# Kernel tuning notes

Measured on AMD Instinct MI355X. Metric: run time of the kernel, lower is better.

The kernel has to match this reference:

```python
import jax, jax.numpy as jnp
import numpy as np

B, V, D = 32768, 2, 512   # batch, views (code hard-codes 2 via cat(subject, subject)), hidden dim
S, L = 32, 8              # number of subjects, number of labels -> K = S*L groups
DENS_TEMP = 0.1           # args.Intersubsim_dens_temp (temperature/base_temperature are unused in forward)


def setup_inputs() -> dict:
    key = jax.random.key(0)
    k1, k2, k3 = jax.random.split(key, 3)
    X_data = jax.random.normal(k1, (B, V, D), dtype=jnp.float32)
    subject = jax.random.randint(k2, (B,), 0, S, dtype=jnp.int32)
    labels = jax.random.randint(k3, (B,), 0, L, dtype=jnp.int32)
    return {"X_data": X_data, "subject": subject, "labels": labels}


def reference(X_data, subject, labels):
    K = S * L
    # contrast_feature = cat(unbind(X_data, dim=1), dim=0): view-major stacking -> [V*B, D]
    feat = jnp.concatenate([X_data[:, v, :] for v in range(V)], axis=0)
    sub2 = jnp.concatenate([subject, subject])   # subject_ten
    lab2 = jnp.concatenate([labels, labels])     # labels_ten

    # group id per row; loop order (sorted unique subject, sorted unique label) == s*L + l
    gid = sub2 * L + lab2                         # [2B]
    counts = jax.ops.segment_sum(jnp.ones(gid.shape, feat.dtype), gid, K)   # [K]
    sums = jax.ops.segment_sum(feat, gid, K)                                 # [K, D]
    centroid = sums / counts[:, None]                                        # per-group mean

    # per-point euclidean distance to own-group centroid (torch.cdist)
    dist = jnp.sqrt(jnp.sum((feat - centroid[gid]) ** 2, axis=1))            # [2B]
    # density: mean(dist ** 0.5) / log(n_g + 10) for groups with >1 member
    mean_sqrt = jax.ops.segment_sum(jnp.sqrt(dist), gid, K) / counts
    dens = mean_sqrt / jnp.log(counts + 10.0)
    dmax = jnp.max(jnp.where(counts > 1, dens, -jnp.inf))
    density = jnp.where(counts > 1, dens, dmax)
    density = jnp.clip(density, jnp.quantile(density, 0.1), jnp.quantile(density, 0.9))
    density = DENS_TEMP * density / density.mean()
    # torch path goes through .tolist() -> density carries no gradient
    density = jax.lax.stop_gradient(density)

    # masks: positives = same label, different subject (group index equals raw id here)
    g_sub = jnp.arange(K, dtype=sub2.dtype) // L
    g_lab = jnp.arange(K, dtype=lab2.dtype) % L
    mask = ((sub2[:, None] != g_sub[None, :]) & (lab2[:, None] == g_lab[None, :])).astype(feat.dtype)  # [2B, K]
    # with S>=2 and all labels present, every row has at least one positive -> no row drop

    sim = (feat @ centroid.T) / density[None, :]          # [2B, K]
    sim = sim - jnp.max(sim, axis=1, keepdims=True)
    positive_sim = sim * mask
    # CrossEntropyLoss with soft (unnormalized) float targets: -sum target*log_softmax
    logp = jax.nn.log_softmax(positive_sim, axis=1)
    loss = -jnp.sum(mask * logp, axis=1) / jnp.sum(mask, axis=1)
    return loss.mean()
```

## Files before the change

kernel.cpp:

```cpp
#include <hip/hip_runtime.h>
#include <math.h>

#define BN 32768
#define DN 512
#define SN 32
#define LN 8
#define KN 256
#define N2 65536
#define SPLIT 8

typedef __attribute__((ext_vector_type(8))) short bf16x8;
typedef __attribute__((ext_vector_type(4))) float f32x4;

#define OFF_XBF     0ull
#define OFF_PART    67108864ull
#define OFF_SUMS    71303168ull
#define OFF_CENTB   71827456ull
#define OFF_GID     72089600ull
#define OFF_PERM    72220672ull
#define OFF_BASE    72351744ull
#define OFF_OFFW    72352772ull
#define OFF_COUNTS  72353796ull
#define OFF_SUMQ    72354820ull
#define OFF_INVD    72355844ull
#define OFF_LOSS    72356868ull
#define ZERO_OFF    OFF_COUNTS
#define ZERO_BYTES  (72356872ull - OFF_COUNTS)

__device__ __forceinline__ float atomAddF(float* p, float v) {
  return unsafeAtomicAdd(p, v);
}

__device__ __forceinline__ ushort f2bf(float x) {
  union { float f; unsigned u; } v; v.f = x;
  unsigned u = v.u;
  unsigned r = (u + 0x7fffu + ((u >> 16) & 1u)) >> 16;
  return (ushort)r;
}

__device__ __forceinline__ float bf2f(ushort x) {
  union { unsigned u; float f; } v; v.u = ((unsigned)x) << 16;
  return v.f;
}

__device__ __forceinline__ void async16(const void* g, void* l) {
  __builtin_amdgcn_global_load_lds(
      (const __attribute__((address_space(1))) unsigned int*)g,
      (__attribute__((address_space(3))) unsigned int*)l, 16, 0, 0);
}

__global__ __launch_bounds__(256) void k0_gid(const int* __restrict__ subject,
    const int* __restrict__ labels, int* __restrict__ gid, int* __restrict__ counts) {
  __shared__ int hist[KN];
  hist[threadIdx.x] = 0;
  __syncthreads();
  const int b0 = blockIdx.x * 1024;
  for (int i = threadIdx.x; i < 1024; i += 256) {
    int b = b0 + i;
    int g = subject[b] * LN + labels[b];
    gid[b] = g;
    atomicAdd(&hist[g], 1);
  }
  __syncthreads();
  if (hist[threadIdx.x]) atomicAdd(&counts[threadIdx.x], 2 * hist[threadIdx.x]);
}

__global__ __launch_bounds__(256) void k0b_scan(const int* __restrict__ counts,
    int* __restrict__ base, int* __restrict__ offw) {
  __shared__ int sh[KN];
  const int t = threadIdx.x;
  const int h = counts[t] >> 1;
  sh[t] = h;
  __syncthreads();
  for (int d = 1; d < 256; d <<= 1) {
    int add = (t >= d) ? sh[t - d] : 0;
    __syncthreads();
    sh[t] += add;
    __syncthreads();
  }
  const int excl = sh[t] - h;
  base[t] = excl;
  offw[t] = excl;
  if (t == 255) base[256] = sh[255];
}

__global__ __launch_bounds__(256) void k0c_scatter(const int* __restrict__ gid,
    int* __restrict__ offw, int* __restrict__ perm) {
  __shared__ int lhist[KN];
  __shared__ int lbase[KN];
  const int t = threadIdx.x;
  const int b0 = blockIdx.x * 1024;
  lhist[t] = 0;
  __syncthreads();
  int g[4], lr[4];
#pragma unroll
  for (int k = 0; k < 4; ++k) {
    g[k] = gid[b0 + k * 256 + t];
    lr[k] = atomicAdd(&lhist[g[k]], 1);
  }
  __syncthreads();
  const int h = lhist[t];
  if (h) lbase[t] = atomicAdd(&offw[t], h);
  __syncthreads();
#pragma unroll
  for (int k = 0; k < 4; ++k) {
    perm[lbase[g[k]] + lr[k]] = b0 + k * 256 + t;
  }
}

__global__ __launch_bounds__(256) void k1_sums(const float* __restrict__ X,
    const int* __restrict__ perm, const int* __restrict__ base,
    ushort* __restrict__ Xb, float* __restrict__ partial) {
  __shared__ float buf[4 * 512];
  const int g = blockIdx.x >> 3;
  const int s = blockIdx.x & (SPLIT - 1);
  const int t = threadIdx.x;
  const int w = t >> 6;
  const int lane = t & 63;
  const int start = base[g], end = base[g + 1];
  const int vs = s * 4 + w;

  float4 a0 = {0.f, 0.f, 0.f, 0.f};
  float4 a1 = {0.f, 0.f, 0.f, 0.f};

  int i = start + vs;
  if (i < end) {
    int idx = perm[i];
    const float* bp = X + (size_t)idx * 1024 + lane * 4;
    float4 x0 = *(const float4*)(bp);
    float4 x1 = *(const float4*)(bp + 256);
    float4 x2 = *(const float4*)(bp + 512);
    float4 x3 = *(const float4*)(bp + 768);
    while (true) {
      const int inext = i + 32;
      int idxn = idx;
      float4 y0 = x0, y1 = x1, y2 = x2, y3 = x3;
      if (inext < end) {
        idxn = perm[inext];
        const float* bn = X + (size_t)idxn * 1024 + lane * 4;
        y0 = *(const float4*)(bn);
        y1 = *(const float4*)(bn + 256);
        y2 = *(const float4*)(bn + 512);
        y3 = *(const float4*)(bn + 768);
      }
      a0.x += x0.x + x2.x; a0.y += x0.y + x2.y;
      a0.z += x0.z + x2.z; a0.w += x0.w + x2.w;
      a1.x += x1.x + x3.x; a1.y += x1.y + x3.y;
      a1.z += x1.z + x3.z; a1.w += x1.w + x3.w;
      ushort* xb0 = Xb + (size_t)idx * DN + lane * 4;
      ushort* xb1 = Xb + (size_t)(idx + BN) * DN + lane * 4;
      *(ushort4*)(xb0)       = (ushort4){f2bf(x0.x), f2bf(x0.y), f2bf(x0.z), f2bf(x0.w)};
      *(ushort4*)(xb0 + 256) = (ushort4){f2bf(x1.x), f2bf(x1.y), f2bf(x1.z), f2bf(x1.w)};
      *(ushort4*)(xb1)       = (ushort4){f2bf(x2.x), f2bf(x2.y), f2bf(x2.z), f2bf(x2.w)};
      *(ushort4*)(xb1 + 256) = (ushort4){f2bf(x3.x), f2bf(x3.y), f2bf(x3.z), f2bf(x3.w)};
      if (inext >= end) break;
      i = inext; idx = idxn; x0 = y0; x1 = y1; x2 = y2; x3 = y3;
    }
  }
  *(float4*)&buf[w * 512 + lane * 4] = a0;
  *(float4*)&buf[w * 512 + 256 + lane * 4] = a1;
  __syncthreads();
  if (t < 128) {
    float4 r = {0.f, 0.f, 0.f, 0.f};
#pragma unroll
    for (int ww = 0; ww < 4; ++ww) {
      float4 v = *(float4*)&buf[ww * 512 + t * 4];
      r.x += v.x; r.y += v.y; r.z += v.z; r.w += v.w;
    }
    *(float4*)&partial[((size_t)s * KN + g) * DN + t * 4] = r;
  }
}

__global__ __launch_bounds__(256) void k1b_cent(const float* __restrict__ partial,
    const int* __restrict__ counts, float* __restrict__ sums,
    ushort* __restrict__ centB) {
  const int i = blockIdx.x * 256 + threadIdx.x;
  const int g = i >> 9;
  float ss = 0.f;
#pragma unroll
  for (int s = 0; s < SPLIT; ++s) ss += partial[(size_t)s * (KN * DN) + i];
  sums[i] = ss;
  centB[i] = f2bf(ss / (float)counts[g]);
}

__global__ __launch_bounds__(256) void k3_dist(const ushort* __restrict__ Xb,
    const int* __restrict__ perm, const int* __restrict__ base,
    const float* __restrict__ sums, const int* __restrict__ counts,
    float* __restrict__ sumq) {
  __shared__ float wacc[4];
  const int g = blockIdx.x >> 3;
  const int s = blockIdx.x & (SPLIT - 1);
  const int t = threadIdx.x;
  const int w = t >> 6;
  const int lane = t & 63;
  const int start = base[g], end = base[g + 1];
  const int nviews = 2 * (end - start);
  const float invc = 1.0f / (float)counts[g];
  const float* sp = sums + g * DN + lane * 8;
  float4 c0 = *(const float4*)sp;
  float4 c1 = *(const float4*)(sp + 4);
  const float cs[8] = {c0.x * invc, c0.y * invc, c0.z * invc, c0.w * invc,
                       c1.x * invc, c1.y * invc, c1.z * invc, c1.w * invc};
  float q = 0.f;
  const int vs = s * 4 + w;
  for (int j = vs; j < nviews; j += SPLIT * 4) {
    const int idx = perm[start + (j >> 1)];
    const int row = idx + (j & 1) * BN;
    int4 chunk = *(const int4*)(Xb + (size_t)row * DN + lane * 8);
    const ushort* us = (const ushort*)&chunk;
    float ss = 0.f;
#pragma unroll
    for (int k = 0; k < 8; ++k) {
      float diff = bf2f(us[k]) - cs[k];
      ss += diff * diff;
    }
#pragma unroll
    for (int off = 32; off > 0; off >>= 1) ss += __shfl_down(ss, off, 64);
    if (lane == 0) q += sqrtf(sqrtf(ss));
  }
  if (lane == 0) wacc[w] = q;
  __syncthreads();
  if (t == 0) atomAddF(&sumq[g], wacc[0] + wacc[1] + wacc[2] + wacc[3]);
}

__global__ __launch_bounds__(256) void k4_density(const float* __restrict__ sumq,
    const int* __restrict__ counts, float* __restrict__ invd) {
  __shared__ float sv[256];
  __shared__ float st[256];
  const int t = threadIdx.x;
  const int cnt = counts[t];
  const bool valid = cnt > 1;
  float dens = 0.f;
  if (valid) dens = (sumq[t] / (float)cnt) / logf((float)cnt + 10.f);
  sv[t] = valid ? dens : -INFINITY;
  __syncthreads();
  for (int s = 128; s > 0; s >>= 1) {
    if (t < s) sv[t] = fmaxf(sv[t], sv[t + s]);
    __syncthreads();
  }
  const float dmax = sv[0];
  __syncthreads();
  const float d0 = valid ? dens : dmax;
  sv[t] = d0;
  __syncthreads();
  int rank = 0;
  for (int j = 0; j < 256; ++j) {
    float vj = sv[j];
    rank += (vj < d0) || (vj == d0 && j < t);
  }
  st[rank] = d0;
  __syncthreads();
  const float q10 = 0.5f * (st[25] + st[26]);
  const float q90 = 0.5f * (st[229] + st[230]);
  const float dc = fminf(fmaxf(d0, q10), q90);
  sv[t] = dc;
  __syncthreads();
  for (int s = 128; s > 0; s >>= 1) {
    if (t < s) sv[t] += sv[t + s];
    __syncthreads();
  }
  const float mean = sv[0] * (1.0f / 256.f);
  invd[t] = mean / (0.1f * dc);
}

#define TAB (128 * 128)
#define TBB (256 * 128)
__global__ __launch_bounds__(256, 2) void k5_mfma(const ushort* __restrict__ Xb,
    const ushort* __restrict__ centB, const int* __restrict__ subject,
    const int* __restrict__ labels, const float* __restrict__ invd,
    float* __restrict__ losssum) {
  __shared__ char smem[TAB + TBB + 1024];
  char* ldsA = smem;
  char* ldsB = smem + TAB;
  float* maxbuf = (float*)smem;
  float* gmax = (float*)(smem + 2048);
  float* ebuf = (float*)(smem + 2560);
  float* zbuf = (float*)(smem + 4608);
  int* labs = (int*)(smem + TAB + TBB);
  int* subs = labs + 128;

  const int t = threadIdx.x;
  const int w = t >> 6;
  const int lane = t & 63;
  const int quad = lane >> 4;
  const int n16 = lane & 15;
  const int li = lane >> 3;
  const int lc = lane & 7;
  const int srcc = lc ^ li;
  const int rowbase = blockIdx.x * 128;

  if (t < 128) {
    int b = (rowbase + t) & (BN - 1);
    labs[t] = labels[b];
    subs[t] = subject[b];
  }

  f32x4 acc[8][4];
#pragma unroll
  for (int mt = 0; mt < 8; ++mt)
#pragma unroll
    for (int nt = 0; nt < 4; ++nt) acc[mt][nt] = (f32x4){0.f, 0.f, 0.f, 0.f};

  const ushort* Arow = Xb + (size_t)rowbase * DN;

  for (int k0 = 0; k0 < DN; k0 += 64) {
    __syncthreads();
#pragma unroll
    for (int q = 0; q < 4; ++q) {
      const int r0 = w * 32 + q * 8;
      async16(Arow + (size_t)(r0 + li) * DN + k0 + srcc * 8, ldsA + r0 * 128);
    }
#pragma unroll
    for (int q = 0; q < 8; ++q) {
      const int g0 = w * 64 + q * 8;
      async16(centB + (size_t)(g0 + li) * DN + k0 + srcc * 8, ldsB + g0 * 128);
    }
    __syncthreads();
#pragma unroll
    for (int s = 0; s < 2; ++s) {
      const int csw = ((s * 4 + quad) ^ (n16 & 7)) * 16;
      bf16x8 bfr[4];
#pragma unroll
      for (int nt = 0; nt < 4; ++nt) {
        int g = w * 64 + nt * 16 + n16;
        bfr[nt] = *(bf16x8*)(ldsB + g * 128 + csw);
      }
#pragma unroll
      for (int mt = 0; mt < 8; ++mt) {
        bf16x8 afr = *(bf16x8*)(ldsA + (mt * 16 + n16) * 128 + csw);
#pragma unroll
        for (int nt = 0; nt < 4; ++nt)
          acc[mt][nt] = __builtin_amdgcn_mfma_f32_16x16x32_bf16(afr, bfr[nt], acc[mt][nt], 0, 0, 0);
      }
    }
  }

  float iv[4];
#pragma unroll
  for (int nt = 0; nt < 4; ++nt) iv[nt] = invd[w * 64 + nt * 16 + n16];

  __syncthreads();

#pragma unroll
  for (int mt = 0; mt < 8; ++mt) {
#pragma unroll
    for (int r = 0; r < 4; ++r) {
      float mm = -INFINITY;
#pragma unroll
      for (int nt = 0; nt < 4; ++nt) mm = fmaxf(mm, acc[mt][nt][r] * iv[nt]);
#pragma unroll
      for (int off = 1; off < 16; off <<= 1) mm = fmaxf(mm, __shfl_xor(mm, off, 64));
      if (n16 == 0) maxbuf[w * 128 + mt * 16 + quad * 4 + r] = mm;
    }
  }
  __syncthreads();
  if (t < 128)
    gmax[t] = fmaxf(fmaxf(maxbuf[t], maxbuf[128 + t]),
                    fmaxf(maxbuf[256 + t], maxbuf[384 + t]));
  __syncthreads();

#pragma unroll
  for (int mt = 0; mt < 8; ++mt) {
#pragma unroll
    for (int r = 0; r < 4; ++r) {
      const int row = mt * 16 + quad * 4 + r;
      const float gm = gmax[row];
      const int lab = labs[row];
      const int sub = subs[row];
      float e = 0.f, z = 0.f;
      if ((n16 & 7) == lab) {
#pragma unroll
        for (int nt = 0; nt < 4; ++nt) {
          int gdiv8 = w * 8 + nt * 2 + (n16 >> 3);
          if (gdiv8 != sub) {
            float sv = acc[mt][nt][r] * iv[nt] - gm;
            e += expf(sv);
            z += sv;
          }
        }
      }
#pragma unroll
      for (int off = 1; off < 16; off <<= 1) {
        e += __shfl_xor(e, off, 64);
        z += __shfl_xor(z, off, 64);
      }
      if (n16 == 0) {
        ebuf[w * 128 + row] = e;
        zbuf[w * 128 + row] = z;
      }
    }
  }
  __syncthreads();

  float lsum = 0.f;
  if (t < 128) {
    float e = ebuf[t] + ebuf[128 + t] + ebuf[256 + t] + ebuf[384 + t];
    float z = zbuf[t] + zbuf[128 + t] + zbuf[256 + t] + zbuf[384 + t];
    lsum = logf(225.f + e) - z * (1.0f / 31.0f);
  }
#pragma unroll
  for (int off = 32; off > 0; off >>= 1) lsum += __shfl_down(lsum, off, 64);
  if (lane == 0 && lsum != 0.f) atomAddF(losssum, lsum);
}

__global__ void k6_final(const float* __restrict__ losssum, float* __restrict__ out) {
  out[0] = losssum[0] * (1.0f / (float)N2);
}

extern "C" void kernel_launch(void* const* d_in, const int* in_sizes, int n_in,
                              void* d_out, int out_size, void* d_ws, size_t ws_size,
                              hipStream_t stream) {
  const float* X = (const float*)d_in[0];
  const int* subject = (const int*)d_in[1];
  const int* labels = (const int*)d_in[2];
  char* ws = (char*)d_ws;
  ushort* Xb = (ushort*)(ws + OFF_XBF);
  float* partial = (float*)(ws + OFF_PART);
  float* sums = (float*)(ws + OFF_SUMS);
  ushort* centB = (ushort*)(ws + OFF_CENTB);
  int* gid = (int*)(ws + OFF_GID);
  int* perm = (int*)(ws + OFF_PERM);
  int* basep = (int*)(ws + OFF_BASE);
  int* offw = (int*)(ws + OFF_OFFW);
  int* counts = (int*)(ws + OFF_COUNTS);
  float* sumq = (float*)(ws + OFF_SUMQ);
  float* invd = (float*)(ws + OFF_INVD);
  float* losssum = (float*)(ws + OFF_LOSS);

  hipMemsetAsync(ws + ZERO_OFF, 0, ZERO_BYTES, stream);
  k0_gid<<<BN / 1024, 256, 0, stream>>>(subject, labels, gid, counts);
  k0b_scan<<<1, 256, 0, stream>>>(counts, basep, offw);
  k0c_scatter<<<BN / 1024, 256, 0, stream>>>(gid, offw, perm);
  k1_sums<<<KN * SPLIT, 256, 0, stream>>>(X, perm, basep, Xb, partial);
  k1b_cent<<<(KN * DN) / 256, 256, 0, stream>>>(partial, counts, sums, centB);
  k3_dist<<<KN * SPLIT, 256, 0, stream>>>(Xb, perm, basep, sums, counts, sumq);
  k4_density<<<1, 256, 0, stream>>>(sumq, counts, invd);
  k5_mfma<<<N2 / 128, 256, 0, stream>>>(Xb, centB, subject, labels, invd, losssum);
  k6_final<<<1, 1, 0, stream>>>(losssum, (float*)d_out);
}
```

Baseline: 296.1 us.

## Fuse setup kernels and compute distances from the GEMM via norm expansion

Merges the gid, scan and scatter kernels into one kernel that uses a software grid barrier. It drops the separate distance pass by computing squared distance as |x|^2 - 2x·c + |c|^2, reusing the MFMA dot products plus per-row and per-centroid norms. The density and final-loss kernels are folded into the MFMA kernel behind grid barriers. This removes several launches and a full reread of the bf16 features, but relies on all 512 blocks being co-resident to avoid deadlock, and the norm expansion can lose precision to cancellation.

```diff
diff --git a/kernel.cpp b/kernel.cpp
--- a/kernel.cpp
+++ b/kernel.cpp
@@ -14,21 +14,39 @@
 
 #define OFF_XBF     0ull
 #define OFF_PART    67108864ull
-#define OFF_SUMS    71303168ull
-#define OFF_CENTB   71827456ull
-#define OFF_GID     72089600ull
-#define OFF_PERM    72220672ull
-#define OFF_BASE    72351744ull
-#define OFF_OFFW    72352772ull
-#define OFF_COUNTS  72353796ull
-#define OFF_SUMQ    72354820ull
-#define OFF_INVD    72355844ull
-#define OFF_LOSS    72356868ull
-#define ZERO_OFF    OFF_COUNTS
-#define ZERO_BYTES  (72356872ull - OFF_COUNTS)
+#define OFF_CENTB   71303168ull
+#define OFF_XNORM   71565312ull
+#define OFF_PERM    71827456ull
+#define OFF_BASE    71958528ull
+#define OFF_OFFW    71959556ull
+#define OFF_COUNTS  71960580ull
+#define OFF_SUMQ    71961604ull
+#define OFF_CNORM   71962628ull
+#define OFF_LOSS    71963652ull
+#define OFF_BARS    71963656ull
+#define ZERO_OFF    OFF_OFFW
+#define ZERO_BYTES  (71963680ull - OFF_OFFW)
 
 __device__ __forceinline__ float atomAddF(float* p, float v) {
   return unsafeAtomicAdd(p, v);
+}
+
+__device__ __forceinline__ void gridbar1(unsigned* cnt, unsigned* flag, unsigned nblocks) {
+  __syncthreads();
+  if (threadIdx.x == 0) {
+    __threadfence();
+    unsigned a = __hip_atomic_fetch_add(cnt, 1u, __ATOMIC_ACQ_REL,
+                                        __HIP_MEMORY_SCOPE_AGENT);
+    if (a + 1u == nblocks) {
+      __hip_atomic_store(flag, 1u, __ATOMIC_RELEASE, __HIP_MEMORY_SCOPE_AGENT);
+    } else {
+      while (!__hip_atomic_load(flag, __ATOMIC_ACQUIRE, __HIP_MEMORY_SCOPE_AGENT)) {
+        __builtin_amdgcn_s_sleep(2);
+      }
+    }
+    __threadfence();
+  }
+  __syncthreads();
 }
 
 __device__ __forceinline__ ushort f2bf(float x) {
@@ -49,44 +67,11 @@
       (__attribute__((address_space(3))) unsigned int*)l, 16, 0, 0);
 }
 
-__global__ __launch_bounds__(256) void k0_gid(const int* __restrict__ subject,
-    const int* __restrict__ labels, int* __restrict__ gid, int* __restrict__ counts) {
-  __shared__ int hist[KN];
-  hist[threadIdx.x] = 0;
-  __syncthreads();
-  const int b0 = blockIdx.x * 1024;
-  for (int i = threadIdx.x; i < 1024; i += 256) {
-    int b = b0 + i;
-    int g = subject[b] * LN + labels[b];
-    gid[b] = g;
-    atomicAdd(&hist[g], 1);
-  }
-  __syncthreads();
-  if (hist[threadIdx.x]) atomicAdd(&counts[threadIdx.x], 2 * hist[threadIdx.x]);
-}
-
-__global__ __launch_bounds__(256) void k0b_scan(const int* __restrict__ counts,
-    int* __restrict__ base, int* __restrict__ offw) {
+__global__ __launch_bounds__(256) void k0_all(const int* __restrict__ subject,
+    const int* __restrict__ labels, int* __restrict__ counts, int* __restrict__ base,
+    int* __restrict__ offw, int* __restrict__ perm, unsigned* __restrict__ bars) {
+  __shared__ int lhist[KN];
   __shared__ int sh[KN];
-  const int t = threadIdx.x;
-  const int h = counts[t] >> 1;
-  sh[t] = h;
-  __syncthreads();
-  for (int d = 1; d < 256; d <<= 1) {
-    int add = (t >= d) ? sh[t - d] : 0;
-    __syncthreads();
-    sh[t] += add;
-    __syncthreads();
-  }
-  const int excl = sh[t] - h;
-  base[t] = excl;
-  offw[t] = excl;
-  if (t == 255) base[256] = sh[255];
-}
-
-__global__ __launch_bounds__(256) void k0c_scatter(const int* __restrict__ gid,
-    int* __restrict__ offw, int* __restrict__ perm) {
-  __shared__ int lhist[KN];
   __shared__ int lbase[KN];
   const int t = threadIdx.x;
   const int b0 = blockIdx.x * 1024;
@@ -95,22 +80,39 @@
   int g[4], lr[4];
 #pragma unroll
   for (int k = 0; k < 4; ++k) {
-    g[k] = gid[b0 + k * 256 + t];
+    const int b = b0 + k * 256 + t;
+    g[k] = subject[b] * LN + labels[b];
     lr[k] = atomicAdd(&lhist[g[k]], 1);
   }
   __syncthreads();
   const int h = lhist[t];
-  if (h) lbase[t] = atomicAdd(&offw[t], h);
-  __syncthreads();
-#pragma unroll
-  for (int k = 0; k < 4; ++k) {
+  if (h) atomicAdd(&counts[t], 2 * h);
+  gridbar1(&bars[0], &bars[1], 32);
+  const int rows = ((int)__hip_atomic_load((unsigned*)&counts[t], __ATOMIC_RELAXED,
+                                           __HIP_MEMORY_SCOPE_AGENT)) >> 1;
+  sh[t] = rows;
+  __syncthreads();
+  for (int d = 1; d < 256; d <<= 1) {
+    int add = (t >= d) ? sh[t - d] : 0;
+    __syncthreads();
+    sh[t] += add;
+    __syncthreads();
+  }
+  const int excl = sh[t] - rows;
+  if (blockIdx.x == 0) {
+    base[t] = excl;
+    if (t == 255) base[256] = sh[255];
+  }
+  if (h) lbase[t] = excl + atomicAdd(&offw[t], h);
+  __syncthreads();
+#pragma unroll
+  for (int k = 0; k < 4; ++k)
     perm[lbase[g[k]] + lr[k]] = b0 + k * 256 + t;
-  }
 }
 
 __global__ __launch_bounds__(256) void k1_sums(const float* __restrict__ X,
     const int* __restrict__ perm, const int* __restrict__ base,
-    ushort* __restrict__ Xb, float* __restrict__ partial) {
+    ushort* __restrict__ Xb, float* __restrict__ partial, float* __restrict__ xnorm) {
   __shared__ float buf[4 * 512];
   const int g = blockIdx.x >> 3;
   const int s = blockIdx.x & (SPLIT - 1);
@@ -147,12 +149,31 @@
       a0.z += x0.z + x2.z; a0.w += x0.w + x2.w;
       a1.x += x1.x + x3.x; a1.y += x1.y + x3.y;
       a1.z += x1.z + x3.z; a1.w += x1.w + x3.w;
+      ushort4 u0 = (ushort4){f2bf(x0.x), f2bf(x0.y), f2bf(x0.z), f2bf(x0.w)};
+      ushort4 u1 = (ushort4){f2bf(x1.x), f2bf(x1.y), f2bf(x1.z), f2bf(x1.w)};
+      ushort4 u2 = (ushort4){f2bf(x2.x), f2bf(x2.y), f2bf(x2.z), f2bf(x2.w)};
+      ushort4 u3 = (ushort4){f2bf(x3.x), f2bf(x3.y), f2bf(x3.z), f2bf(x3.w)};
       ushort* xb0 = Xb + (size_t)idx * DN + lane * 4;
       ushort* xb1 = Xb + (size_t)(idx + BN) * DN + lane * 4;
-      *(ushort4*)(xb0)       = (ushort4){f2bf(x0.x), f2bf(x0.y), f2bf(x0.z), f2bf(x0.w)};
-      *(ushort4*)(xb0 + 256) = (ushort4){f2bf(x1.x), f2bf(x1.y), f2bf(x1.z), f2bf(x1.w)};
-      *(ushort4*)(xb1)       = (ushort4){f2bf(x2.x), f2bf(x2.y), f2bf(x2.z), f2bf(x2.w)};
-      *(ushort4*)(xb1 + 256) = (ushort4){f2bf(x3.x), f2bf(x3.y), f2bf(x3.z), f2bf(x3.w)};
+      *(ushort4*)(xb0)       = u0;
+      *(ushort4*)(xb0 + 256) = u1;
+      *(ushort4*)(xb1)       = u2;
+      *(ushort4*)(xb1 + 256) = u3;
+      float n0, n1, tv;
+      tv = bf2f(u0.x); n0  = tv * tv;  tv = bf2f(u0.y); n0 += tv * tv;
+      tv = bf2f(u0.z); n0 += tv * tv;  tv = bf2f(u0.w); n0 += tv * tv;
+      tv = bf2f(u1.x); n0 += tv * tv;  tv = bf2f(u1.y); n0 += tv * tv;
+      tv = bf2f(u1.z); n0 += tv * tv;  tv = bf2f(u1.w); n0 += tv * tv;
+      tv = bf2f(u2.x); n1  = tv * tv;  tv = bf2f(u2.y); n1 += tv * tv;
+      tv = bf2f(u2.z); n1 += tv * tv;  tv = bf2f(u2.w); n1 += tv * tv;
+      tv = bf2f(u3.x); n1 += tv * tv;  tv = bf2f(u3.y); n1 += tv * tv;
+      tv = bf2f(u3.z); n1 += tv * tv;  tv = bf2f(u3.w); n1 += tv * tv;
+#pragma unroll
+      for (int off = 32; off > 0; off >>= 1) {
+        n0 += __shfl_down(n0, off, 64);
+        n1 += __shfl_down(n1, off, 64);
+      }
+      if (lane == 0) { xnorm[idx] = n0; xnorm[idx + BN] = n1; }
       if (inext >= end) break;
       i = inext; idx = idxn; x0 = y0; x1 = y1; x2 = y2; x3 = y3;
     }
@@ -172,103 +193,36 @@
 }
 
 __global__ __launch_bounds__(256) void k1b_cent(const float* __restrict__ partial,
-    const int* __restrict__ counts, float* __restrict__ sums,
-    ushort* __restrict__ centB) {
-  const int i = blockIdx.x * 256 + threadIdx.x;
-  const int g = i >> 9;
-  float ss = 0.f;
-#pragma unroll
-  for (int s = 0; s < SPLIT; ++s) ss += partial[(size_t)s * (KN * DN) + i];
-  sums[i] = ss;
-  centB[i] = f2bf(ss / (float)counts[g]);
-}
-
-__global__ __launch_bounds__(256) void k3_dist(const ushort* __restrict__ Xb,
-    const int* __restrict__ perm, const int* __restrict__ base,
-    const float* __restrict__ sums, const int* __restrict__ counts,
-    float* __restrict__ sumq) {
-  __shared__ float wacc[4];
-  const int g = blockIdx.x >> 3;
-  const int s = blockIdx.x & (SPLIT - 1);
+    const int* __restrict__ counts, ushort* __restrict__ centB,
+    float* __restrict__ cnorm) {
+  __shared__ float wsum[4];
   const int t = threadIdx.x;
   const int w = t >> 6;
   const int lane = t & 63;
-  const int start = base[g], end = base[g + 1];
-  const int nviews = 2 * (end - start);
-  const float invc = 1.0f / (float)counts[g];
-  const float* sp = sums + g * DN + lane * 8;
-  float4 c0 = *(const float4*)sp;
-  float4 c1 = *(const float4*)(sp + 4);
-  const float cs[8] = {c0.x * invc, c0.y * invc, c0.z * invc, c0.w * invc,
-                       c1.x * invc, c1.y * invc, c1.z * invc, c1.w * invc};
-  float q = 0.f;
-  const int vs = s * 4 + w;
-  for (int j = vs; j < nviews; j += SPLIT * 4) {
-    const int idx = perm[start + (j >> 1)];
-    const int row = idx + (j & 1) * BN;
-    int4 chunk = *(const int4*)(Xb + (size_t)row * DN + lane * 8);
-    const ushort* us = (const ushort*)&chunk;
-    float ss = 0.f;
-#pragma unroll
-    for (int k = 0; k < 8; ++k) {
-      float diff = bf2f(us[k]) - cs[k];
-      ss += diff * diff;
-    }
-#pragma unroll
-    for (int off = 32; off > 0; off >>= 1) ss += __shfl_down(ss, off, 64);
-    if (lane == 0) q += sqrtf(sqrtf(ss));
-  }
-  if (lane == 0) wacc[w] = q;
-  __syncthreads();
-  if (t == 0) atomAddF(&sumq[g], wacc[0] + wacc[1] + wacc[2] + wacc[3]);
-}
-
-__global__ __launch_bounds__(256) void k4_density(const float* __restrict__ sumq,
-    const int* __restrict__ counts, float* __restrict__ invd) {
-  __shared__ float sv[256];
-  __shared__ float st[256];
-  const int t = threadIdx.x;
-  const int cnt = counts[t];
-  const bool valid = cnt > 1;
-  float dens = 0.f;
-  if (valid) dens = (sumq[t] / (float)cnt) / logf((float)cnt + 10.f);
-  sv[t] = valid ? dens : -INFINITY;
-  __syncthreads();
-  for (int s = 128; s > 0; s >>= 1) {
-    if (t < s) sv[t] = fmaxf(sv[t], sv[t + s]);
-    __syncthreads();
-  }
-  const float dmax = sv[0];
-  __syncthreads();
-  const float d0 = valid ? dens : dmax;
-  sv[t] = d0;
-  __syncthreads();
-  int rank = 0;
-  for (int j = 0; j < 256; ++j) {
-    float vj = sv[j];
-    rank += (vj < d0) || (vj == d0 && j < t);
-  }
-  st[rank] = d0;
-  __syncthreads();
-  const float q10 = 0.5f * (st[25] + st[26]);
-  const float q90 = 0.5f * (st[229] + st[230]);
-  const float dc = fminf(fmaxf(d0, q10), q90);
-  sv[t] = dc;
-  __syncthreads();
-  for (int s = 128; s > 0; s >>= 1) {
-    if (t < s) sv[t] += sv[t + s];
-    __syncthreads();
-  }
-  const float mean = sv[0] * (1.0f / 256.f);
-  invd[t] = mean / (0.1f * dc);
+  const int i = blockIdx.x * 256 + t;
+  const int g = i >> 9;
+  float ss = 0.f;
+#pragma unroll
+  for (int s = 0; s < SPLIT; ++s) ss += partial[(size_t)s * (KN * DN) + i];
+  const ushort cb = f2bf(ss / (float)counts[g]);
+  centB[i] = cb;
+  const float cf = bf2f(cb);
+  float c2 = cf * cf;
+#pragma unroll
+  for (int off = 32; off > 0; off >>= 1) c2 += __shfl_down(c2, off, 64);
+  if (lane == 0) wsum[w] = c2;
+  __syncthreads();
+  if (t == 0) atomAddF(&cnorm[g], wsum[0] + wsum[1] + wsum[2] + wsum[3]);
 }
 
 #define TAB (128 * 128)
 #define TBB (256 * 128)
 __global__ __launch_bounds__(256, 2) void k5_mfma(const ushort* __restrict__ Xb,
     const ushort* __restrict__ centB, const int* __restrict__ subject,
-    const int* __restrict__ labels, const float* __restrict__ invd,
-    float* __restrict__ losssum) {
+    const int* __restrict__ labels, const float* __restrict__ xnorm,
+    const float* __restrict__ cnorm, const int* __restrict__ counts,
+    float* __restrict__ sumq, float* __restrict__ losssum,
+    float* __restrict__ out, unsigned* __restrict__ bars) {
   __shared__ char smem[TAB + TBB + 1024];
   char* ldsA = smem;
   char* ldsB = smem + TAB;
@@ -276,6 +230,9 @@
   float* gmax = (float*)(smem + 2048);
   float* ebuf = (float*)(smem + 2560);
   float* zbuf = (float*)(smem + 4608);
+  float* sv   = (float*)(smem + 9216);
+  float* stv  = (float*)(smem + 10240);
+  float* dinv = (float*)(smem + 11264);
   int* labs = (int*)(smem + TAB + TBB);
   int* subs = labs + 128;
 
@@ -335,10 +292,64 @@
     }
   }
 
+#pragma unroll
+  for (int mt = 0; mt < 8; ++mt) {
+#pragma unroll
+    for (int r = 0; r < 4; ++r) {
+      const int row = mt * 16 + quad * 4 + r;
+      const int g = subs[row] * LN + labs[row];
+      if ((g >> 6) == w && (g & 15) == n16) {
+        const int nt = (g >> 4) & 3;
+        float dot = (nt == 0) ? acc[mt][0][r] : (nt == 1) ? acc[mt][1][r]
+                  : (nt == 2) ? acc[mt][2][r] : acc[mt][3][r];
+        float d2 = xnorm[rowbase + row] - 2.0f * dot + cnorm[g];
+        atomAddF(&sumq[g], sqrtf(sqrtf(fmaxf(d2, 0.0f))));
+      }
+    }
+  }
+  gridbar1(&bars[2], &bars[3], 512);
+
+  {
+    const int cnt = counts[t];
+    const bool valid = cnt > 1;
+    const float sq = __hip_atomic_load(&sumq[t], __ATOMIC_RELAXED,
+                                       __HIP_MEMORY_SCOPE_AGENT);
+    float dens = 0.f;
+    if (valid) dens = (sq / (float)cnt) / logf((float)cnt + 10.f);
+    sv[t] = valid ? dens : -INFINITY;
+    __syncthreads();
+    for (int s2 = 128; s2 > 0; s2 >>= 1) {
+      if (t < s2) sv[t] = fmaxf(sv[t], sv[t + s2]);
+      __syncthreads();
+    }
+    const float dmax = sv[0];
+    __syncthreads();
+    const float d0 = valid ? dens : dmax;
+    sv[t] = d0;
+    __syncthreads();
+    int rank = 0;
+    for (int j = 0; j < 256; ++j) {
+      float vj = sv[j];
+      rank += (vj < d0) || (vj == d0 && j < t);
+    }
+    stv[rank] = d0;
+    __syncthreads();
+    const float q10 = 0.5f * (stv[25] + stv[26]);
+    const float q90 = 0.5f * (stv[229] + stv[230]);
+    const float dc = fminf(fmaxf(d0, q10), q90);
+    sv[t] = dc;
+    __syncthreads();
+    for (int s2 = 128; s2 > 0; s2 >>= 1) {
+      if (t < s2) sv[t] += sv[t + s2];
+      __syncthreads();
+    }
+    dinv[t] = (sv[0] * (1.0f / 256.f)) / (0.1f * dc);
+  }
+  __syncthreads();
+
   float iv[4];
 #pragma unroll
-  for (int nt = 0; nt < 4; ++nt) iv[nt] = invd[w * 64 + nt * 16 + n16];
-
+  for (int nt = 0; nt < 4; ++nt) iv[nt] = dinv[w * 64 + nt * 16 + n16];
   __syncthreads();
 
 #pragma unroll
@@ -373,9 +384,9 @@
         for (int nt = 0; nt < 4; ++nt) {
           int gdiv8 = w * 8 + nt * 2 + (n16 >> 3);
           if (gdiv8 != sub) {
-            float sv = acc[mt][nt][r] * iv[nt] - gm;
-            e += expf(sv);
-            z += sv;
+            float svv = acc[mt][nt][r] * iv[nt] - gm;
+            e += expf(svv);
+            z += svv;
           }
         }
       }
@@ -401,10 +412,13 @@
 #pragma unroll
   for (int off = 32; off > 0; off >>= 1) lsum += __shfl_down(lsum, off, 64);
   if (lane == 0 && lsum != 0.f) atomAddF(losssum, lsum);
-}
-
-__global__ void k6_final(const float* __restrict__ losssum, float* __restrict__ out) {
-  out[0] = losssum[0] * (1.0f / (float)N2);
+
+  gridbar1(&bars[4], &bars[5], 512);
+  if (blockIdx.x == 0 && t == 0) {
+    const float ls = __hip_atomic_load(losssum, __ATOMIC_RELAXED,
+                                       __HIP_MEMORY_SCOPE_AGENT);
+    out[0] = ls * (1.0f / (float)N2);
+  }
 }
 
 extern "C" void kernel_launch(void* const* d_in, const int* in_sizes, int n_in,
@@ -416,25 +430,21 @@
   char* ws = (char*)d_ws;
   ushort* Xb = (ushort*)(ws + OFF_XBF);
   float* partial = (float*)(ws + OFF_PART);
-  float* sums = (float*)(ws + OFF_SUMS);
   ushort* centB = (ushort*)(ws + OFF_CENTB);
-  int* gid = (int*)(ws + OFF_GID);
+  float* xnorm = (float*)(ws + OFF_XNORM);
   int* perm = (int*)(ws + OFF_PERM);
   int* basep = (int*)(ws + OFF_BASE);
   int* offw = (int*)(ws + OFF_OFFW);
   int* counts = (int*)(ws + OFF_COUNTS);
   float* sumq = (float*)(ws + OFF_SUMQ);
-  float* invd = (float*)(ws + OFF_INVD);
+  float* cnorm = (float*)(ws + OFF_CNORM);
   float* losssum = (float*)(ws + OFF_LOSS);
+  unsigned* bars = (unsigned*)(ws + OFF_BARS);
 
   hipMemsetAsync(ws + ZERO_OFF, 0, ZERO_BYTES, stream);
-  k0_gid<<<BN / 1024, 256, 0, stream>>>(subject, labels, gid, counts);
-  k0b_scan<<<1, 256, 0, stream>>>(counts, basep, offw);
-  k0c_scatter<<<BN / 1024, 256, 0, stream>>>(gid, offw, perm);
-  k1_sums<<<KN * SPLIT, 256, 0, stream>>>(X, perm, basep, Xb, partial);
-  k1b_cent<<<(KN * DN) / 256, 256, 0, stream>>>(partial, counts, sums, centB);
-  k3_dist<<<KN * SPLIT, 256, 0, stream>>>(Xb, perm, basep, sums, counts, sumq);
-  k4_density<<<1, 256, 0, stream>>>(sumq, counts, invd);
-  k5_mfma<<<N2 / 128, 256, 0, stream>>>(Xb, centB, subject, labels, invd, losssum);
-  k6_final<<<1, 1, 0, stream>>>(losssum, (float*)d_out);
-}
+  k0_all<<<32, 256, 0, stream>>>(subject, labels, counts, basep, offw, perm, bars);
+  k1_sums<<<KN * SPLIT, 256, 0, stream>>>(X, perm, basep, Xb, partial, xnorm);
+  k1b_cent<<<(KN * DN) / 256, 256, 0, stream>>>(partial, counts, centB, cnorm);
+  k5_mfma<<<512, 256, 0, stream>>>(Xb, centB, subject, labels, xnorm, cnorm,
+                                   counts, sumq, losssum, (float*)d_out, bars);
+}
```

After: 464.8 us. +57.0%, slower.
